# Performance work log

Hardware: AMD Instinct MI355X
Metric: run time of the kernel (lower is better)

## Reference

```python
import jax, jax.numpy as jnp
import numpy as np

B, S, DM, H, FF = 2, 2048, 1024, 16, 4096
DH = DM // H
EPS = 1e-5


def setup_inputs() -> dict:
    key = jax.random.key(0)
    ks = jax.random.split(key, 16)
    s = 0.02
    return {
        "x": jax.random.normal(ks[0], (B, S, DM), jnp.float32),
        "mask": jnp.ones((B, S), jnp.int32),
        "Wq": jax.random.normal(ks[1], (DM, DM), jnp.float32) * s,
        "bq": jnp.zeros((DM,), jnp.float32),
        "Wk": jax.random.normal(ks[2], (DM, DM), jnp.float32) * s,
        "bk": jnp.zeros((DM,), jnp.float32),
        "Wv": jax.random.normal(ks[3], (DM, DM), jnp.float32) * s,
        "bv": jnp.zeros((DM,), jnp.float32),
        "Wo": jax.random.normal(ks[4], (DM, DM), jnp.float32) * s,
        "bo": jnp.zeros((DM,), jnp.float32),
        "W1": jax.random.normal(ks[5], (DM, FF), jnp.float32) * s,
        "b1": jnp.zeros((FF,), jnp.float32),
        "W2": jax.random.normal(ks[6], (FF, DM), jnp.float32) * s,
        "b2": jnp.zeros((DM,), jnp.float32),
        "g1": jnp.ones((DM,), jnp.float32),
        "beta1": jnp.zeros((DM,), jnp.float32),
        "g2": jnp.ones((DM,), jnp.float32),
        "beta2": jnp.zeros((DM,), jnp.float32),
    }


def _layer_norm(x, g, b):
    mu = jnp.mean(x, axis=-1, keepdims=True)
    var = jnp.var(x, axis=-1, keepdims=True)
    return (x - mu) * jax.lax.rsqrt(var + EPS) * g + b


def reference(x, mask, Wq, bq, Wk, bk, Wv, bv, Wo, bo, W1, b1, W2, b2, g1, beta1, g2, beta2):
    # --- hollow multi-head attention ---
    q = (x @ Wq + bq).reshape(B, S, H, DH)
    k = (x @ Wk + bk).reshape(B, S, H, DH)
    v = (x @ Wv + bv).reshape(B, S, H, DH)
    scores = jnp.einsum("bqhd,bkhd->bhqk", q, k) / jnp.sqrt(jnp.float32(DH))
    # triu(diag=1) and tril(diag=-1) masks kill everything off-diagonal
    diag = jnp.eye(S, dtype=bool)  # [S, S]
    scores = jnp.where(diag[None, None], scores, -jnp.inf)
    attn = jax.nn.softmax(scores, axis=-1)
    out = jnp.einsum("bhqk,bkhd->bqhd", attn, v).reshape(B, S, DM)
    attn_out = out @ Wo + bo
    # --- residual + LN1 ---
    h = _layer_norm(x + attn_out, g1, beta1)
    # --- FFN ---
    ff = jax.nn.relu(h @ W1 + b1) @ W2 + b2
    # --- residual + LN2 ---
    return _layer_norm(h + ff, g2, beta2)
```

## Files before the change

kernel.cpp:

```cpp
#include <hip/hip_runtime.h>
#include <stdint.h>

typedef __bf16 bf16x8 __attribute__((ext_vector_type(8)));
typedef float f32x4 __attribute__((ext_vector_type(4)));

__device__ __forceinline__ uint16_t f2bf(float f) {
  union { float f; uint32_t u; } c; c.f = f;
  uint32_t u = c.u;
  u += 0x7fffu + ((u >> 16) & 1u);
  return (uint16_t)(u >> 16);
}
__device__ __forceinline__ float bf2f(uint16_t u) {
  union { uint32_t u; float f; } c; c.u = (uint32_t)u << 16; return c.f;
}

__global__ void cvt_bf16_kernel(const float* __restrict__ in, uint16_t* __restrict__ out, int n4) {
  int i = blockIdx.x * blockDim.x + threadIdx.x;
  if (i >= n4) return;
  float4 v = reinterpret_cast<const float4*>(in)[i];
  ushort4 o;
  o.x = f2bf(v.x); o.y = f2bf(v.y); o.z = f2bf(v.z); o.w = f2bf(v.w);
  reinterpret_cast<ushort4*>(out)[i] = o;
}

__global__ void transpose_cvt_kernel(const float* __restrict__ in, uint16_t* __restrict__ out,
                                     int R, int C) {
  __shared__ float t[32][33];
  const int tx = threadIdx.x, ty = threadIdx.y;
  const int c0 = blockIdx.x * 32, r0 = blockIdx.y * 32;
#pragma unroll
  for (int i = 0; i < 4; ++i)
    t[ty + i * 8][tx] = in[(size_t)(r0 + ty + i * 8) * C + (c0 + tx)];
  __syncthreads();
#pragma unroll
  for (int i = 0; i < 4; ++i)
    out[(size_t)(c0 + ty + i * 8) * R + (r0 + tx)] = f2bf(t[tx][ty + i * 8]);
}

__global__ void bc_kernel(const float* __restrict__ bv, const float* __restrict__ Wo,
                          const float* __restrict__ bo, float* __restrict__ bc) {
  const int jl = threadIdx.x & 31, kg = threadIdx.x >> 5;
  const int j = blockIdx.x * 32 + jl;
  float s = 0.f;
  const int k0 = kg * 128;
  for (int k = k0; k < k0 + 128; ++k)
    s += bv[k] * Wo[(size_t)k * 1024 + j];
  __shared__ float red[8][32];
  red[kg][jl] = s;
  __syncthreads();
  if (kg == 0) {
    float t = bo[j];
#pragma unroll
    for (int q = 0; q < 8; ++q) t += red[q][jl];
    bc[j] = t;
  }
}

constexpr int BM = 128, BN = 128, BK = 64;

template <int MODE>
__launch_bounds__(256, 2)
__global__ void gemm2ph_kernel(const uint16_t* __restrict__ A, const uint16_t* __restrict__ Bt,
                               const float* __restrict__ bias, const float* __restrict__ res,
                               void* __restrict__ out, int M, int N, int Klen, int lda, int ldb) {
  __shared__ uint16_t sAB[2][2][BM * BK];
  const int tid  = threadIdx.x;
  const int lane = tid & 63;
  const int wave = tid >> 6;

  const int nwg = gridDim.x * gridDim.y;
  int wg = blockIdx.y * gridDim.x + blockIdx.x;
  wg = (wg & 7) * (nwg >> 3) + (wg >> 3);
  const int bx = wg % gridDim.x, by = wg / gridDim.x;
  const int m0 = by * BM, n0 = bx * BN;

  const int wm = (wave >> 1) * 64;
  const int wn = (wave & 1) * 64;

  f32x4 acc[4][4] = {};

  const int srow = tid >> 3;
  const int scol = ((tid & 7) ^ (srow & 7)) * 8;
  const uint16_t* ga[4];
  const uint16_t* gb[4];
  uint32_t loff[4];
#pragma unroll
  for (int g = 0; g < 4; ++g) {
    const int row = srow + 32 * g;
    ga[g] = A + (size_t)(m0 + row) * lda + scol;
    gb[g] = Bt + (size_t)(n0 + row) * ldb + scol;
    loff[g] = (uint32_t)(tid + g * 256) * 8;
  }

  const int fr = lane & 15;
  const int hi = lane >> 4;
  const int rx = fr & 7;

  const int nk = Klen / BK;

#define STAGE2(buf, kt)                                                                   \
  {                                                                                       \
    _Pragma("unroll")                                                                     \
    for (int g = 0; g < 4; ++g) {                                                         \
      __builtin_amdgcn_global_load_lds(                                                   \
          (const __attribute__((address_space(1))) uint32_t*)(ga[g] + (size_t)(kt) * BK), \
          (__attribute__((address_space(3))) uint32_t*)(&sAB[buf][0][loff[g]]), 16, 0, 0);\
      __builtin_amdgcn_global_load_lds(                                                   \
          (const __attribute__((address_space(1))) uint32_t*)(gb[g] + (size_t)(kt) * BK), \
          (__attribute__((address_space(3))) uint32_t*)(&sAB[buf][1][loff[g]]), 16, 0, 0);\
    }                                                                                     \
  }

  STAGE2(0, 0);
  __syncthreads();

  int cur = 0;
  for (int kt = 0; kt < nk; ++kt) {
    if (kt + 1 < nk) STAGE2(cur ^ 1, kt + 1);
    const uint16_t* pA = &sAB[cur][0][0];
    const uint16_t* pB = &sAB[cur][1][0];
    bf16x8 af[4][2], bb[4][2];
#pragma unroll
    for (int m = 0; m < 4; ++m)
#pragma unroll
      for (int ks = 0; ks < 2; ++ks) {
        const int slot = (ks * 4 + hi) ^ rx;
        af[m][ks] = *reinterpret_cast<const bf16x8*>(pA + (wm + m * 16 + fr) * BK + slot * 8);
        bb[m][ks] = *reinterpret_cast<const bf16x8*>(pB + (wn + m * 16 + fr) * BK + slot * 8);
      }
#pragma unroll
    for (int ks = 0; ks < 2; ++ks)
#pragma unroll
      for (int m = 0; m < 4; ++m)
#pragma unroll
        for (int n = 0; n < 4; ++n)
          acc[m][n] = __builtin_amdgcn_mfma_f32_16x16x32_bf16(af[m][ks], bb[n][ks], acc[m][n], 0, 0, 0);
    __syncthreads();
    cur ^= 1;
  }
#undef STAGE2

  const int cn  = lane & 15;
  const int cm4 = (lane >> 4) * 4;
#pragma unroll
  for (int m = 0; m < 4; ++m) {
#pragma unroll
    for (int n = 0; n < 4; ++n) {
      const int gm = m0 + wm + m * 16 + cm4;
      const int gn = n0 + wn + n * 16 + cn;
      const float bbv = bias ? bias[gn] : 0.f;
#pragma unroll
      for (int r = 0; r < 4; ++r) {
        const size_t idx = (size_t)(gm + r) * N + gn;
        const float vv = acc[m][n][r] + bbv;
        if constexpr (MODE == 0) {
          ((uint16_t*)out)[idx] = f2bf(vv);
        } else {
          ((float*)out)[idx] = vv + res[idx];
        }
      }
    }
  }
}

template <int MODE>
__launch_bounds__(512, 2)
__global__ void gemm8ph_kernel(const uint16_t* __restrict__ A, const uint16_t* __restrict__ Bt,
                               const float* __restrict__ bias, void* __restrict__ out,
                               int M, int N, int Klen, int lda, int ldb) {
  extern __shared__ uint16_t lds[];
  const int tid  = threadIdx.x;
  const int lane = tid & 63;
  const int wave = tid >> 6;

  const int nwg = gridDim.x * gridDim.y;
  int wg = blockIdx.y * gridDim.x + blockIdx.x;
  wg = (wg & 7) * (nwg >> 3) + (wg >> 3);
  const int bx = wg % gridDim.x, by = wg / gridDim.x;
  const int m0 = by * 256, n0 = bx * 256;

  const int z = blockIdx.z;
  A  += (size_t)z * Klen;
  Bt += (size_t)z * Klen;

  const int wm = (wave >> 2) * 128;
  const int wn = (wave & 3) * 64;

  f32x4 acc[8][4] = {};

  const int R0 = tid >> 2;
  const int sg = ((tid & 3) ^ (((tid >> 2) ^ (tid >> 4)) & 3)) * 8;
  const uint16_t* gA0 = A + (size_t)(m0 + R0) * lda + sg;
  const uint16_t* gA1 = A + (size_t)(m0 + R0 + 128) * lda + sg;
  const uint16_t* gB0 = Bt + (size_t)(n0 + R0) * ldb + sg;
  const uint16_t* gB1 = Bt + (size_t)(n0 + R0 + 128) * ldb + sg;

  const int nk = Klen / 64;

#define STAGE8(T, R)                                                                        \
  if ((T) < nk) {                                                                           \
    const uint16_t* s0 = (((R) & 1) ? gA0 : gB0) + (size_t)(T) * 64 + ((R) >> 1) * 32;      \
    const uint16_t* s1 = (((R) & 1) ? gA1 : gB1) + (size_t)(T) * 64 + ((R) >> 1) * 32;      \
    uint16_t* d = lds + (((T) & 1) * 32768 + (R) * 8192);                                   \
    __builtin_amdgcn_global_load_lds(                                                       \
        (const __attribute__((address_space(1))) uint32_t*)s0,                              \
        (__attribute__((address_space(3))) uint32_t*)(d + (size_t)tid * 8), 16, 0, 0);      \
    __builtin_amdgcn_global_load_lds(                                                       \
        (const __attribute__((address_space(1))) uint32_t*)s1,                              \
        (__attribute__((address_space(3))) uint32_t*)(d + (size_t)(tid + 512) * 8), 16, 0, 0); \
  }

  const int fr = lane & 15;
  const int hi = lane >> 4;
  const int g  = (fr ^ (fr >> 2)) & 3;
  const int laneA = wm * 32 + fr * 32 + ((hi ^ g) * 8);
  const int laneB = wn * 32 + fr * 32 + ((hi ^ g) * 8);

  STAGE8(0, 0); STAGE8(0, 1); STAGE8(0, 2); STAGE8(0, 3);
  asm volatile("s_waitcnt vmcnt(4)" ::: "memory");
  STAGE8(1, 0); STAGE8(1, 1); STAGE8(1, 2);
  asm volatile("s_waitcnt vmcnt(6)" ::: "memory");
  __builtin_amdgcn_s_barrier();

#define MFMA16(MB)                                                        \
  __builtin_amdgcn_s_setprio(1);                                          \
  _Pragma("unroll") for (int m = 0; m < 4; ++m)                           \
    _Pragma("unroll") for (int n = 0; n < 4; ++n)                         \
      acc[m + (MB)][n] = __builtin_amdgcn_mfma_f32_16x16x32_bf16(         \
          aq[m], bq[n], acc[m + (MB)][n], 0, 0, 0);                       \
  __builtin_amdgcn_s_setprio(0);

  for (int k = 0; k < nk; ++k) {
    const uint16_t* bufp = lds + (k & 1) * 32768;
    bf16x8 aq[4], bq[4];
#pragma unroll
    for (int n = 0; n < 4; ++n) bq[n] = *reinterpret_cast<const bf16x8*>(bufp + 0 * 8192 + laneB + n * 512);
#pragma unroll
    for (int m = 0; m < 4; ++m) aq[m] = *reinterpret_cast<const bf16x8*>(bufp + 1 * 8192 + laneA + m * 512);
    STAGE8(k + 1, 3);
    __builtin_amdgcn_s_barrier();
    asm volatile("s_waitcnt lgkmcnt(0)" ::: "memory");
    MFMA16(0);
    __builtin_amdgcn_s_barrier();
#pragma unroll
    for (int m = 0; m < 4; ++m) aq[m] = *reinterpret_cast<const bf16x8*>(bufp + 1 * 8192 + laneA + (m + 4) * 512);
    STAGE8(k + 2, 0);
    __builtin_amdgcn_s_barrier();
    asm volatile("s_waitcnt lgkmcnt(0)" ::: "memory");
    MFMA16(4);
    __builtin_amdgcn_s_barrier();
#pragma unroll
    for (int n = 0; n < 4; ++n) bq[n] = *reinterpret_cast<const bf16x8*>(bufp + 2 * 8192 + laneB + n * 512);
#pragma unroll
    for (int m = 0; m < 4; ++m) aq[m] = *reinterpret_cast<const bf16x8*>(bufp + 3 * 8192 + laneA + m * 512);
    STAGE8(k + 2, 1);
    __builtin_amdgcn_s_barrier();
    asm volatile("s_waitcnt lgkmcnt(0)" ::: "memory");
    MFMA16(0);
    __builtin_amdgcn_s_barrier();
#pragma unroll
    for (int m = 0; m < 4; ++m) aq[m] = *reinterpret_cast<const bf16x8*>(bufp + 3 * 8192 + laneA + (m + 4) * 512);
    STAGE8(k + 2, 2);
    if (k < nk - 2) { asm volatile("s_waitcnt vmcnt(6)" ::: "memory"); }
    else            { asm volatile("s_waitcnt vmcnt(0)" ::: "memory"); }
    __builtin_amdgcn_s_barrier();
    asm volatile("s_waitcnt lgkmcnt(0)" ::: "memory");
    MFMA16(4);
    __builtin_amdgcn_s_barrier();
  }
#undef MFMA16
#undef STAGE8

  const int cn  = lane & 15;
  const int cm4 = (lane >> 4) * 4;
  uint16_t* outp = (uint16_t*)out;
  if constexpr (MODE == 1) outp += (size_t)z * M * N;
  float bias_n[4];
  if constexpr (MODE == 0) {
#pragma unroll
    for (int n = 0; n < 4; ++n) bias_n[n] = bias[n0 + wn + n * 16 + cn];
  }
#pragma unroll
  for (int m = 0; m < 8; ++m) {
#pragma unroll
    for (int n = 0; n < 4; ++n) {
      const int gm = m0 + wm + m * 16 + cm4;
      const int gn = n0 + wn + n * 16 + cn;
#pragma unroll
      for (int r = 0; r < 4; ++r) {
        const size_t idx = (size_t)(gm + r) * N + gn;
        if constexpr (MODE == 0) {
          outp[idx] = f2bf(fmaxf(acc[m][n][r] + bias_n[n], 0.f));
        } else {
          outp[idx] = f2bf(acc[m][n][r]);
        }
      }
    }
  }
}

__global__ void ln1_kernel(const float* __restrict__ in,
                           const float* __restrict__ g,
                           const float* __restrict__ b,
                           uint16_t* __restrict__ outb) {
  const int row = blockIdx.x;
  const int t = threadIdx.x;
  const float4 v = reinterpret_cast<const float4*>(in + (size_t)row * 1024)[t];
  float s  = v.x + v.y + v.z + v.w;
  float s2 = v.x * v.x + v.y * v.y + v.z * v.z + v.w * v.w;
#pragma unroll
  for (int o = 32; o > 0; o >>= 1) { s += __shfl_down(s, o); s2 += __shfl_down(s2, o); }
  __shared__ float red[8];
  const int lane = t & 63, wave = t >> 6;
  if (lane == 0) { red[wave] = s; red[4 + wave] = s2; }
  __syncthreads();
  const float S  = red[0] + red[1] + red[2] + red[3];
  const float S2 = red[4] + red[5] + red[6] + red[7];
  const float mu  = S * (1.f / 1024.f);
  const float var = S2 * (1.f / 1024.f) - mu * mu;
  const float rs  = rsqrtf(var + 1e-5f);
  const float4 gg = reinterpret_cast<const float4*>(g)[t];
  const float4 bb = reinterpret_cast<const float4*>(b)[t];
  ushort4 ob;
  ob.x = f2bf((v.x - mu) * rs * gg.x + bb.x);
  ob.y = f2bf((v.y - mu) * rs * gg.y + bb.y);
  ob.z = f2bf((v.z - mu) * rs * gg.z + bb.z);
  ob.w = f2bf((v.w - mu) * rs * gg.w + bb.w);
  reinterpret_cast<ushort4*>(outb + (size_t)row * 1024)[t] = ob;
}

__global__ void ln2_kernel(const uint16_t* __restrict__ pp, size_t pstride,
                           const uint16_t* __restrict__ hb, const float* __restrict__ b2,
                           const float* __restrict__ g, const float* __restrict__ be,
                           float* __restrict__ out) {
  const int row = blockIdx.x;
  const int t = threadIdx.x;
  const size_t base = (size_t)row * 1024;
  const ushort4 h4 = reinterpret_cast<const ushort4*>(hb + base)[t];
  const float4 c2 = reinterpret_cast<const float4*>(b2)[t];
  float4 v;
  v.x = c2.x + bf2f(h4.x); v.y = c2.y + bf2f(h4.y);
  v.z = c2.z + bf2f(h4.z); v.w = c2.w + bf2f(h4.w);
#pragma unroll
  for (int zz = 0; zz < 4; ++zz) {
    const ushort4 p4 = reinterpret_cast<const ushort4*>(pp + zz * pstride + base)[t];
    v.x += bf2f(p4.x); v.y += bf2f(p4.y); v.z += bf2f(p4.z); v.w += bf2f(p4.w);
  }
  float s  = v.x + v.y + v.z + v.w;
  float s2 = v.x * v.x + v.y * v.y + v.z * v.z + v.w * v.w;
#pragma unroll
  for (int o = 32; o > 0; o >>= 1) { s += __shfl_down(s, o); s2 += __shfl_down(s2, o); }
  __shared__ float red[8];
  const int lane = t & 63, wave = t >> 6;
  if (lane == 0) { red[wave] = s; red[4 + wave] = s2; }
  __syncthreads();
  const float S  = red[0] + red[1] + red[2] + red[3];
  const float S2 = red[4] + red[5] + red[6] + red[7];
  const float mu  = S * (1.f / 1024.f);
  const float var = S2 * (1.f / 1024.f) - mu * mu;
  const float rs  = rsqrtf(var + 1e-5f);
  const float4 gg = reinterpret_cast<const float4*>(g)[t];
  const float4 bb = reinterpret_cast<const float4*>(be)[t];
  float4 o;
  o.x = (v.x - mu) * rs * gg.x + bb.x;
  o.y = (v.y - mu) * rs * gg.y + bb.y;
  o.z = (v.z - mu) * rs * gg.z + bb.z;
  o.w = (v.w - mu) * rs * gg.w + bb.w;
  reinterpret_cast<float4*>(out + base)[t] = o;
}

extern "C" void kernel_launch(void* const* d_in, const int* in_sizes, int n_in,
                              void* d_out, int out_size, void* d_ws, size_t ws_size,
                              hipStream_t stream) {
  const float* x   = (const float*)d_in[0];
  const float* Wv  = (const float*)d_in[6];
  const float* bv  = (const float*)d_in[7];
  const float* Wo  = (const float*)d_in[8];
  const float* bo  = (const float*)d_in[9];
  const float* W1  = (const float*)d_in[10];
  const float* b1  = (const float*)d_in[11];
  const float* W2  = (const float*)d_in[12];
  const float* b2  = (const float*)d_in[13];
  const float* g1  = (const float*)d_in[14];
  const float* be1 = (const float*)d_in[15];
  const float* g2  = (const float*)d_in[16];
  const float* be2 = (const float*)d_in[17];
  float* out = (float*)d_out;

  constexpr int M = 4096, DM = 1024, FF = 4096;

  char* p = (char*)d_ws;
  auto alloc = [&](size_t bytes) {
    char* r = p;
    p += (bytes + 255) & ~(size_t)255;
    return r;
  };
  uint16_t* xb  = (uint16_t*)alloc((size_t)M * DM * 2);
  uint16_t* wvb = (uint16_t*)alloc((size_t)DM * DM * 2);
  uint16_t* woT = (uint16_t*)alloc((size_t)DM * DM * 2);
  uint16_t* w1t = (uint16_t*)alloc((size_t)FF * DM * 2);
  uint16_t* w2t = (uint16_t*)alloc((size_t)DM * FF * 2);
  uint16_t* wcT = (uint16_t*)alloc((size_t)DM * DM * 2);
  float*    bc  = (float*)   alloc((size_t)DM * 4);
  float*    r1  = (float*)   alloc((size_t)M * DM * 4);
  uint16_t* hb  = (uint16_t*)alloc((size_t)M * DM * 2);
  uint16_t* tb  = (uint16_t*)alloc((size_t)M * FF * 2);
  uint16_t* pp  = (uint16_t*)alloc((size_t)4 * M * DM * 2);

  (void)hipFuncSetAttribute(reinterpret_cast<const void*>(gemm8ph_kernel<0>),
                            hipFuncAttributeMaxDynamicSharedMemorySize, 131072);
  (void)hipFuncSetAttribute(reinterpret_cast<const void*>(gemm8ph_kernel<1>),
                            hipFuncAttributeMaxDynamicSharedMemorySize, 131072);

  const dim3 tb32(32, 8);

  cvt_bf16_kernel<<<M * DM / 4 / 256, 256, 0, stream>>>(x, xb, M * DM / 4);
  cvt_bf16_kernel<<<DM * DM / 4 / 256, 256, 0, stream>>>(Wv, wvb, DM * DM / 4);
  transpose_cvt_kernel<<<dim3(DM / 32, DM / 32), tb32, 0, stream>>>(Wo, woT, DM, DM);
  transpose_cvt_kernel<<<dim3(FF / 32, DM / 32), tb32, 0, stream>>>(W1, w1t, DM, FF);
  transpose_cvt_kernel<<<dim3(DM / 32, FF / 32), tb32, 0, stream>>>(W2, w2t, FF, DM);
  bc_kernel<<<32, 256, 0, stream>>>(bv, Wo, bo, bc);

  gemm2ph_kernel<0><<<dim3(DM / BN, DM / BM), 256, 0, stream>>>(
      woT, wvb, nullptr, nullptr, wcT, DM, DM, DM, DM, DM);
  gemm2ph_kernel<1><<<dim3(DM / BN, M / BM), 256, 0, stream>>>(
      xb, wcT, bc, x, r1, M, DM, DM, DM, DM);
  ln1_kernel<<<M, 256, 0, stream>>>(r1, g1, be1, hb);
  gemm8ph_kernel<0><<<dim3(FF / 256, M / 256), 512, 131072, stream>>>(
      hb, w1t, b1, tb, M, FF, DM, DM, DM);
  gemm8ph_kernel<1><<<dim3(DM / 256, M / 256, 4), 512, 131072, stream>>>(
      tb, w2t, nullptr, pp, M, DM, FF / 4, FF, FF);
  ln2_kernel<<<M, 256, 0, stream>>>(pp, (size_t)M * DM, hb, b2, g2, be2, out);
}
```

Baseline: 162.0 us.

## Fuse prep kernels into one launch and restructure 256x256 GEMM LDS staging

Merges the six preprocessing launches (bf16 casts, transposes, folded bias) into one prep_kernel, with branches chosen by block index, to cut launch overhead. Reworks the 8-wave GEMM's shared-memory layout into 64-row units with an 8-way XOR swizzle and full-K rows. It also changes the staging order so the A and B tiles for the next step are prefetched in four phases with adjusted vmcnt waits and sched_barriers. The goal is fewer bank conflicts and better overlap of global-to-LDS loads with MFMA, at the risk of getting the waitcnt accounting wrong.

```diff
diff --git a/kernel.cpp b/kernel.cpp
--- a/kernel.cpp
+++ b/kernel.cpp
@@ -14,46 +14,66 @@
   union { uint32_t u; float f; } c; c.u = (uint32_t)u << 16; return c.f;
 }
 
-__global__ void cvt_bf16_kernel(const float* __restrict__ in, uint16_t* __restrict__ out, int n4) {
-  int i = blockIdx.x * blockDim.x + threadIdx.x;
-  if (i >= n4) return;
+__device__ __forceinline__ void cvt_body(const float* __restrict__ in,
+                                         uint16_t* __restrict__ out, int i) {
   float4 v = reinterpret_cast<const float4*>(in)[i];
   ushort4 o;
   o.x = f2bf(v.x); o.y = f2bf(v.y); o.z = f2bf(v.z); o.w = f2bf(v.w);
   reinterpret_cast<ushort4*>(out)[i] = o;
 }
 
-__global__ void transpose_cvt_kernel(const float* __restrict__ in, uint16_t* __restrict__ out,
-                                     int R, int C) {
-  __shared__ float t[32][33];
-  const int tx = threadIdx.x, ty = threadIdx.y;
-  const int c0 = blockIdx.x * 32, r0 = blockIdx.y * 32;
+__global__ void prep_kernel(const float* __restrict__ x, const float* __restrict__ Wv,
+                            const float* __restrict__ Wo, const float* __restrict__ W1,
+                            const float* __restrict__ W2, const float* __restrict__ bv,
+                            const float* __restrict__ bo,
+                            uint16_t* __restrict__ xb, uint16_t* __restrict__ wvb,
+                            uint16_t* __restrict__ woT, uint16_t* __restrict__ w1t,
+                            uint16_t* __restrict__ w2t, float* __restrict__ bc) {
+  __shared__ float tsh[32][33];
+  __shared__ float red[8][32];
+  int b = blockIdx.x;
+  const int t = threadIdx.x;
+  if (b < 4096) { cvt_body(x, xb, b * 256 + t); return; }
+  b -= 4096;
+  if (b < 1024) { cvt_body(Wv, wvb, b * 256 + t); return; }
+  b -= 1024;
+
+  const float* tin = nullptr; uint16_t* tout = nullptr;
+  int R = 0, C = 0, bx = 0, by = 0;
+  if (b < 1024) {
+    tin = Wo; tout = woT; R = 1024; C = 1024; bx = b & 31; by = b >> 5;
+  } else if (b < 1024 + 4096) {
+    const int bb = b - 1024;
+    tin = W1; tout = w1t; R = 1024; C = 4096; bx = bb & 127; by = bb >> 7;
+  } else if (b < 1024 + 8192) {
+    const int bb = b - (1024 + 4096);
+    tin = W2; tout = w2t; R = 4096; C = 1024; bx = bb & 31; by = bb >> 5;
+  } else {
+    const int jb = b - (1024 + 8192);
+    const int jl = t & 31, kg = t >> 5;
+    const int j = jb * 32 + jl;
+    float s = 0.f;
+    const int k0 = kg * 128;
+    for (int k = k0; k < k0 + 128; ++k) s += bv[k] * Wo[(size_t)k * 1024 + j];
+    red[kg][jl] = s;
+    __syncthreads();
+    if (kg == 0) {
+      float acc = bo[j];
+#pragma unroll
+      for (int q = 0; q < 8; ++q) acc += red[q][jl];
+      bc[j] = acc;
+    }
+    return;
+  }
+  const int tx = t & 31, ty = t >> 5;
+  const int c0 = bx * 32, r0 = by * 32;
 #pragma unroll
   for (int i = 0; i < 4; ++i)
-    t[ty + i * 8][tx] = in[(size_t)(r0 + ty + i * 8) * C + (c0 + tx)];
+    tsh[ty + i * 8][tx] = tin[(size_t)(r0 + ty + i * 8) * C + (c0 + tx)];
   __syncthreads();
 #pragma unroll
   for (int i = 0; i < 4; ++i)
-    out[(size_t)(c0 + ty + i * 8) * R + (r0 + tx)] = f2bf(t[tx][ty + i * 8]);
-}
-
-__global__ void bc_kernel(const float* __restrict__ bv, const float* __restrict__ Wo,
-                          const float* __restrict__ bo, float* __restrict__ bc) {
-  const int jl = threadIdx.x & 31, kg = threadIdx.x >> 5;
-  const int j = blockIdx.x * 32 + jl;
-  float s = 0.f;
-  const int k0 = kg * 128;
-  for (int k = k0; k < k0 + 128; ++k)
-    s += bv[k] * Wo[(size_t)k * 1024 + j];
-  __shared__ float red[8][32];
-  red[kg][jl] = s;
-  __syncthreads();
-  if (kg == 0) {
-    float t = bo[j];
-#pragma unroll
-    for (int q = 0; q < 8; ++q) t += red[q][jl];
-    bc[j] = t;
-  }
+    tout[(size_t)(c0 + ty + i * 8) * R + (r0 + tx)] = f2bf(tsh[tx][ty + i * 8]);
 }
 
 constexpr int BM = 128, BN = 128, BK = 64;
@@ -188,87 +208,109 @@
 
   f32x4 acc[8][4] = {};
 
-  const int R0 = tid >> 2;
-  const int sg = ((tid & 3) ^ (((tid >> 2) ^ (tid >> 4)) & 3)) * 8;
-  const uint16_t* gA0 = A + (size_t)(m0 + R0) * lda + sg;
-  const uint16_t* gA1 = A + (size_t)(m0 + R0 + 128) * lda + sg;
-  const uint16_t* gB0 = Bt + (size_t)(n0 + R0) * ldb + sg;
-  const uint16_t* gB1 = Bt + (size_t)(n0 + R0 + 128) * ldb + sg;
+  const int srw = tid >> 3;
+  const int sp  = tid & 7;
+  const uint16_t* gu[8];
+#pragma unroll
+  for (int u = 0; u < 8; ++u) {
+    const int key = (srw ^ (srw >> 3) ^ u) & 7;
+    const uint16_t* base = (u < 4) ? A + (size_t)(m0 + u * 64) * lda
+                                   : Bt + (size_t)(n0 + (u - 4) * 64) * ldb;
+    const int ld = (u < 4) ? lda : ldb;
+    gu[u] = base + (size_t)srw * ld + ((sp ^ key) * 8);
+  }
 
   const int nk = Klen / 64;
 
-#define STAGE8(T, R)                                                                        \
-  if ((T) < nk) {                                                                           \
-    const uint16_t* s0 = (((R) & 1) ? gA0 : gB0) + (size_t)(T) * 64 + ((R) >> 1) * 32;      \
-    const uint16_t* s1 = (((R) & 1) ? gA1 : gB1) + (size_t)(T) * 64 + ((R) >> 1) * 32;      \
-    uint16_t* d = lds + (((T) & 1) * 32768 + (R) * 8192);                                   \
-    __builtin_amdgcn_global_load_lds(                                                       \
-        (const __attribute__((address_space(1))) uint32_t*)s0,                              \
-        (__attribute__((address_space(3))) uint32_t*)(d + (size_t)tid * 8), 16, 0, 0);      \
-    __builtin_amdgcn_global_load_lds(                                                       \
-        (const __attribute__((address_space(1))) uint32_t*)s1,                              \
-        (__attribute__((address_space(3))) uint32_t*)(d + (size_t)(tid + 512) * 8), 16, 0, 0); \
+#define STAGE8(T, U)                                                                          \
+  if ((T) < nk) {                                                                             \
+    __builtin_amdgcn_global_load_lds(                                                         \
+        (const __attribute__((address_space(1))) uint32_t*)(gu[U] + (size_t)(T) * 64),        \
+        (__attribute__((address_space(3))) uint32_t*)(lds + ((T) & 1) * 32768 + (U) * 4096 +  \
+                                                      tid * 8),                               \
+        16, 0, 0);                                                                            \
   }
 
   const int fr = lane & 15;
   const int hi = lane >> 4;
-  const int g  = (fr ^ (fr >> 2)) & 3;
-  const int laneA = wm * 32 + fr * 32 + ((hi ^ g) * 8);
-  const int laneB = wn * 32 + fr * 32 + ((hi ^ g) * 8);
-
-  STAGE8(0, 0); STAGE8(0, 1); STAGE8(0, 2); STAGE8(0, 3);
+  int aoff[8];
+#pragma unroll
+  for (int m = 0; m < 8; ++m) {
+    const int u = (wm >> 6) + (m >> 2);
+    const int R = (m & 3) * 16 + fr;
+    const int key = (R ^ (R >> 3) ^ u) & 7;
+    aoff[m] = u * 4096 + R * 64 + ((hi ^ key) * 8);
+  }
+  int boff[4];
+#pragma unroll
+  for (int n = 0; n < 4; ++n) {
+    const int u = 4 + (wn >> 6);
+    const int R = n * 16 + fr;
+    const int key = (R ^ (R >> 3) ^ u) & 7;
+    boff[n] = u * 4096 + R * 64 + ((hi ^ key) * 8);
+  }
+
+  STAGE8(0, 0); STAGE8(0, 2); STAGE8(0, 1); STAGE8(0, 3);
+  STAGE8(0, 4); STAGE8(0, 5); STAGE8(0, 6); STAGE8(0, 7);
+  STAGE8(1, 4); STAGE8(1, 5); STAGE8(1, 6); STAGE8(1, 7);
   asm volatile("s_waitcnt vmcnt(4)" ::: "memory");
-  STAGE8(1, 0); STAGE8(1, 1); STAGE8(1, 2);
-  asm volatile("s_waitcnt vmcnt(6)" ::: "memory");
   __builtin_amdgcn_s_barrier();
 
-#define MFMA16(MB)                                                        \
-  __builtin_amdgcn_s_setprio(1);                                          \
-  _Pragma("unroll") for (int m = 0; m < 4; ++m)                           \
-    _Pragma("unroll") for (int n = 0; n < 4; ++n)                         \
-      acc[m + (MB)][n] = __builtin_amdgcn_mfma_f32_16x16x32_bf16(         \
-          aq[m], bq[n], acc[m + (MB)][n], 0, 0, 0);                       \
+#define LD8(off) (*reinterpret_cast<const bf16x8*>(bufp + (off)))
+#define PHASE_MFMA(q)                                                         \
+  __builtin_amdgcn_s_setprio(1);                                              \
+  _Pragma("unroll") for (int ks = 0; ks < 2; ++ks)                            \
+    _Pragma("unroll") for (int mm = 0; mm < 2; ++mm)                          \
+      _Pragma("unroll") for (int n = 0; n < 4; ++n)                           \
+        acc[2 * (q) + mm][n] = __builtin_amdgcn_mfma_f32_16x16x32_bf16(       \
+            aq[mm][ks], bq[n][ks], acc[2 * (q) + mm][n], 0, 0, 0);            \
   __builtin_amdgcn_s_setprio(0);
 
   for (int k = 0; k < nk; ++k) {
     const uint16_t* bufp = lds + (k & 1) * 32768;
-    bf16x8 aq[4], bq[4];
-#pragma unroll
-    for (int n = 0; n < 4; ++n) bq[n] = *reinterpret_cast<const bf16x8*>(bufp + 0 * 8192 + laneB + n * 512);
-#pragma unroll
-    for (int m = 0; m < 4; ++m) aq[m] = *reinterpret_cast<const bf16x8*>(bufp + 1 * 8192 + laneA + m * 512);
-    STAGE8(k + 1, 3);
+    bf16x8 bq[4][2], aq[2][2];
+#pragma unroll
+    for (int n = 0; n < 4; ++n) { bq[n][0] = LD8(boff[n]); bq[n][1] = LD8(boff[n] ^ 32); }
+#pragma unroll
+    for (int mm = 0; mm < 2; ++mm) { aq[mm][0] = LD8(aoff[mm]); aq[mm][1] = LD8(aoff[mm] ^ 32); }
+    STAGE8(k + 1, 0); STAGE8(k + 1, 2);
     __builtin_amdgcn_s_barrier();
     asm volatile("s_waitcnt lgkmcnt(0)" ::: "memory");
-    MFMA16(0);
-    __builtin_amdgcn_s_barrier();
-#pragma unroll
-    for (int m = 0; m < 4; ++m) aq[m] = *reinterpret_cast<const bf16x8*>(bufp + 1 * 8192 + laneA + (m + 4) * 512);
-    STAGE8(k + 2, 0);
+    __builtin_amdgcn_sched_barrier(0);
+    PHASE_MFMA(0);
+    __builtin_amdgcn_s_barrier();
+#pragma unroll
+    for (int mm = 0; mm < 2; ++mm) { aq[mm][0] = LD8(aoff[2 + mm]); aq[mm][1] = LD8(aoff[2 + mm] ^ 32); }
+    STAGE8(k + 1, 1); STAGE8(k + 1, 3);
+    if (k < nk - 1) { asm volatile("s_waitcnt vmcnt(8)" ::: "memory"); }
+    else            { asm volatile("s_waitcnt vmcnt(0)" ::: "memory"); }
     __builtin_amdgcn_s_barrier();
     asm volatile("s_waitcnt lgkmcnt(0)" ::: "memory");
-    MFMA16(4);
-    __builtin_amdgcn_s_barrier();
-#pragma unroll
-    for (int n = 0; n < 4; ++n) bq[n] = *reinterpret_cast<const bf16x8*>(bufp + 2 * 8192 + laneB + n * 512);
-#pragma unroll
-    for (int m = 0; m < 4; ++m) aq[m] = *reinterpret_cast<const bf16x8*>(bufp + 3 * 8192 + laneA + m * 512);
-    STAGE8(k + 2, 1);
+    __builtin_amdgcn_sched_barrier(0);
+    PHASE_MFMA(1);
+    __builtin_amdgcn_s_barrier();
+#pragma unroll
+    for (int mm = 0; mm < 2; ++mm) { aq[mm][0] = LD8(aoff[4 + mm]); aq[mm][1] = LD8(aoff[4 + mm] ^ 32); }
+    STAGE8(k + 2, 4); STAGE8(k + 2, 5);
     __builtin_amdgcn_s_barrier();
     asm volatile("s_waitcnt lgkmcnt(0)" ::: "memory");
-    MFMA16(0);
-    __builtin_amdgcn_s_barrier();
-#pragma unroll
-    for (int m = 0; m < 4; ++m) aq[m] = *reinterpret_cast<const bf16x8*>(bufp + 3 * 8192 + laneA + (m + 4) * 512);
-    STAGE8(k + 2, 2);
-    if (k < nk - 2) { asm volatile("s_waitcnt vmcnt(6)" ::: "memory"); }
-    else            { asm volatile("s_waitcnt vmcnt(0)" ::: "memory"); }
+    __builtin_amdgcn_sched_barrier(0);
+    PHASE_MFMA(2);
+    __builtin_amdgcn_s_barrier();
+#pragma unroll
+    for (int mm = 0; mm < 2; ++mm) { aq[mm][0] = LD8(aoff[6 + mm]); aq[mm][1] = LD8(aoff[6 + mm] ^ 32); }
+    STAGE8(k + 2, 6); STAGE8(k + 2, 7);
+    if (k < nk - 2)      { asm volatile("s_waitcnt vmcnt(6)" ::: "memory"); }
+    else if (k == nk - 2){ asm volatile("s_waitcnt vmcnt(2)" ::: "memory"); }
+    else                 { asm volatile("s_waitcnt vmcnt(0)" ::: "memory"); }
     __builtin_amdgcn_s_barrier();
     asm volatile("s_waitcnt lgkmcnt(0)" ::: "memory");
-    MFMA16(4);
-    __builtin_amdgcn_s_barrier();
-  }
-#undef MFMA16
+    __builtin_amdgcn_sched_barrier(0);
+    PHASE_MFMA(3);
+    __builtin_amdgcn_s_barrier();
+  }
+#undef PHASE_MFMA
+#undef LD8
 #undef STAGE8
 
   const int cn  = lane & 15;
@@ -412,14 +454,8 @@
   (void)hipFuncSetAttribute(reinterpret_cast<const void*>(gemm8ph_kernel<1>),
                             hipFuncAttributeMaxDynamicSharedMemorySize, 131072);
 
-  const dim3 tb32(32, 8);
-
-  cvt_bf16_kernel<<<M * DM / 4 / 256, 256, 0, stream>>>(x, xb, M * DM / 4);
-  cvt_bf16_kernel<<<DM * DM / 4 / 256, 256, 0, stream>>>(Wv, wvb, DM * DM / 4);
-  transpose_cvt_kernel<<<dim3(DM / 32, DM / 32), tb32, 0, stream>>>(Wo, woT, DM, DM);
-  transpose_cvt_kernel<<<dim3(FF / 32, DM / 32), tb32, 0, stream>>>(W1, w1t, DM, FF);
-  transpose_cvt_kernel<<<dim3(DM / 32, FF / 32), tb32, 0, stream>>>(W2, w2t, FF, DM);
-  bc_kernel<<<32, 256, 0, stream>>>(bv, Wo, bo, bc);
+  prep_kernel<<<4096 + 1024 + 1024 + 4096 + 4096 + 32, 256, 0, stream>>>(
+      x, Wv, Wo, W1, W2, bv, bo, xb, wvb, woT, w1t, w2t, bc);
 
   gemm2ph_kernel<0><<<dim3(DM / BN, DM / BM), 256, 0, stream>>>(
       woT, wvb, nullptr, nullptr, wcT, DM, DM, DM, DM, DM);
```

Result: faster. 156.1 us (-3.7%).
